# Kernel tuning notes

Hardware: AMD Instinct MI355X
Metric: run time of the kernel (lower is better)

## Reference

```python
import jax, jax.numpy as jnp
import numpy as np

B, T, INPUT_DIM = 4, 2048, 256
D_MODEL = 512                       # hidden_dim // 2
EXPAND = 2
D_INNER = D_MODEL * EXPAND          # 1024
HEADDIM = 128                       # _pick_headdim(1024)
NHEADS = D_INNER // HEADDIM         # 8
DSTATE = 16
DCONV = 4
NLAYERS = 4
CONV_DIM = D_INNER + 2 * DSTATE            # 1056
D_IN_PROJ = 2 * D_INNER + 2 * DSTATE + NHEADS  # 2088
EPS = 1e-5


def _dir_params(key):
    ks = jax.random.split(key, 5)
    return dict(
        in_w=jax.random.normal(ks[0], (NLAYERS, D_IN_PROJ, D_MODEL)) * 0.02,
        conv_w=jax.random.normal(ks[1], (NLAYERS, CONV_DIM, DCONV)) * 0.1,
        conv_b=jnp.zeros((NLAYERS, CONV_DIM)),
        dt_bias=jnp.log(jnp.expm1(jax.random.uniform(ks[2], (NLAYERS, NHEADS), minval=1e-3, maxval=0.1))),
        A_log=jnp.log(jax.random.uniform(ks[3], (NLAYERS, NHEADS), minval=1.0, maxval=16.0)),
        D=jnp.ones((NLAYERS, NHEADS)),
        rms_w=jnp.ones((NLAYERS, D_INNER)),
        out_w=jax.random.normal(ks[4], (NLAYERS, D_MODEL, D_INNER)) * 0.02,
    )


def setup_inputs():
    key = jax.random.key(0)
    kx, ke, kf, kb = jax.random.split(key, 4)
    inp = {
        "x": jax.random.normal(kx, (B, T, INPUT_DIM), dtype=jnp.float32),
        "embed_w": jax.random.normal(ke, (D_MODEL, INPUT_DIM)) * 0.02,
        "embed_b": jnp.zeros((D_MODEL,)),
        "ln1_w": jnp.ones((D_MODEL,)), "ln1_b": jnp.zeros((D_MODEL,)),
        "lnout_w": jnp.ones((2 * D_MODEL,)), "lnout_b": jnp.zeros((2 * D_MODEL,)),
    }
    for tag, p in (("f", _dir_params(kf)), ("b", _dir_params(kb))):
        for k, v in p.items():
            inp[f"{k}_{tag}"] = v
    return inp


def _silu(x):
    return x * jax.nn.sigmoid(x)


def _layernorm(x, w, b):
    m = jnp.mean(x, -1, keepdims=True)
    v = jnp.mean((x - m) ** 2, -1, keepdims=True)
    return (x - m) * jax.lax.rsqrt(v + EPS) * w + b


def _mamba2(h, in_w, conv_w, conv_b, dt_bias, A_log, Dh, rms_w, out_w):
    """One Mamba2 (SSD) block: in_proj -> causal depthwise conv -> selective scan
    -> gated RMSNorm -> out_proj. Sequential scan is math-equivalent to the
    chunked SSD kernel."""
    Bb, Tt, _ = h.shape
    zxbcdt = jnp.einsum('btd,ed->bte', h, in_w)
    z = zxbcdt[..., :D_INNER]
    xBC = zxbcdt[..., D_INNER:D_INNER + CONV_DIM]
    dt = zxbcdt[..., D_INNER + CONV_DIM:]                      # [B,T,H]
    # causal depthwise conv over time (kernel DCONV), then silu
    xc = jax.lax.conv_general_dilated(
        jnp.transpose(xBC, (0, 2, 1)), conv_w[:, None, :], (1,),
        [(DCONV - 1, 0)], feature_group_count=CONV_DIM)
    xBC = _silu(jnp.transpose(xc, (0, 2, 1)) + conv_b)
    xs = xBC[..., :D_INNER].reshape(Bb, Tt, NHEADS, HEADDIM)   # [B,T,H,P]
    Bm = xBC[..., D_INNER:D_INNER + DSTATE]                    # [B,T,N]
    Cm = xBC[..., D_INNER + DSTATE:]                           # [B,T,N]
    dt = jax.nn.softplus(dt + dt_bias)                         # [B,T,H]
    dA = jnp.exp(dt * (-jnp.exp(A_log)))                       # [B,T,H]
    xdt = xs * dt[..., None]                                   # [B,T,H,P]
    tm = lambda a: jnp.moveaxis(a, 1, 0)                       # time-major

    def step(s, inp):
        dA_t, xdt_t, B_t, C_t = inp
        s = dA_t[:, :, None, None] * s + xdt_t[..., None] * B_t[:, None, None, :]
        return s, jnp.einsum('bhpn,bn->bhp', s, C_t)

    s0 = jnp.zeros((Bb, NHEADS, HEADDIM, DSTATE), h.dtype)
    _, ys = jax.lax.scan(step, s0, (tm(dA), tm(xdt), tm(Bm), tm(Cm)))
    y = jnp.moveaxis(ys, 0, 1) + Dh[None, None, :, None] * xs
    y = y.reshape(Bb, Tt, D_INNER)
    g = y * _silu(z)                                           # gated RMSNorm (norm after gate)
    g = g * jax.lax.rsqrt(jnp.mean(g * g, -1, keepdims=True) + EPS) * rms_w
    return jnp.einsum('bti,oi->bto', g, out_w)


def _forward(x, embed_w, embed_b, ln1_w, ln1_b, lnout_w, lnout_b,
             in_w_f, conv_w_f, conv_b_f, dt_bias_f, A_log_f, D_f, rms_w_f, out_w_f,
             in_w_b, conv_w_b, conv_b_b, dt_bias_b, A_log_b, D_b, rms_w_b, out_w_b):
    h = _layernorm(jnp.einsum('bti,oi->bto', x, embed_w) + embed_b, ln1_w, ln1_b)
    h_f, h_b = h, h[:, ::-1]
    for i in range(NLAYERS):
        h_f = _mamba2(h_f, in_w_f[i], conv_w_f[i], conv_b_f[i], dt_bias_f[i],
                      A_log_f[i], D_f[i], rms_w_f[i], out_w_f[i]) + h_f
    for i in range(NLAYERS):
        h_b = _mamba2(h_b, in_w_b[i], conv_w_b[i], conv_b_b[i], dt_bias_b[i],
                      A_log_b[i], D_b[i], rms_w_b[i], out_w_b[i]) + h_b
    out = jnp.concatenate([h_f, h_b[:, ::-1]], axis=-1)        # [B,T,2*D_MODEL]
    return _layernorm(out, lnout_w, lnout_b)


def reference(x, embed_w, embed_b, ln1_w, ln1_b, lnout_w, lnout_b,
              in_w_f, conv_w_f, conv_b_f, dt_bias_f, A_log_f, D_f, rms_w_f, out_w_f,
              in_w_b, conv_w_b, conv_b_b, dt_bias_b, A_log_b, D_b, rms_w_b, out_w_b):
    return _forward(x, embed_w, embed_b, ln1_w, ln1_b, lnout_w, lnout_b,
                    in_w_f, conv_w_f, conv_b_f, dt_bias_f, A_log_f, D_f, rms_w_f, out_w_f,
                    in_w_b, conv_w_b, conv_b_b, dt_bias_b, A_log_b, D_b, rms_w_b, out_w_b)
```

## Files before the change

### kernel.cpp

```cpp
#include <hip/hip_runtime.h>
#include <hip/hip_bf16.h>
#include <math.h>

#define BB 4
#define TT 2048
#define BT 8192
#define DM 512
#define DI 1024
#define NH 8
#define HD 128
#define DS 16
#define CONVD 1056
#define DPROJ 2088
#define NL 4
#define CL 128
#define NCH 16
#define NE 131072

typedef __hip_bfloat16 bf16;
typedef __attribute__((ext_vector_type(8))) short short8;
typedef __attribute__((ext_vector_type(4))) short short4v;
typedef __attribute__((ext_vector_type(4))) float f32x4;

#define AS_G __attribute__((address_space(1)))
#define AS_L __attribute__((address_space(3)))

static __device__ __forceinline__ float b2f_raw(short v){
  union { unsigned u; float f; } c; c.u = ((unsigned)(unsigned short)v) << 16; return c.f;
}
static __device__ __forceinline__ float u32_lo(unsigned u){
  union { unsigned u; float f; } c; c.u = u << 16; return c.f;
}
static __device__ __forceinline__ float u32_hi(unsigned u){
  union { unsigned u; float f; } c; c.u = u & 0xffff0000u; return c.f;
}
static __device__ __forceinline__ unsigned pack_bf16x2(float a, float b){
  unsigned lo = __bfloat16_as_ushort(__float2bfloat16(a));
  unsigned hi = __bfloat16_as_ushort(__float2bfloat16(b));
  return lo | (hi << 16);
}

static __device__ __forceinline__ void red2(float& a, float& b, float* sb){
  #pragma unroll
  for (int o = 32; o; o >>= 1){ a += __shfl_down(a, o); b += __shfl_down(b, o); }
  int w = threadIdx.x >> 6;
  if ((threadIdx.x & 63) == 0){ sb[w] = a; sb[4+w] = b; }
  __syncthreads();
  a = sb[0]+sb[1]+sb[2]+sb[3];
  b = sb[4]+sb[5]+sb[6]+sb[7];
}

__global__ __launch_bounds__(256) void detect_dtype(const void* x, int* flagp){
  __shared__ int cnt;
  if (threadIdx.x == 0) cnt = 0;
  __syncthreads();
  const bf16* p = (const bf16*)x;
  int bad = 0;
  for (int i = threadIdx.x; i < 32768; i += 256){
    float v = __bfloat162float(p[i]);
    if (!isfinite(v) || fabsf(v) > 1e4f) bad++;
  }
  atomicAdd(&cnt, bad);
  __syncthreads();
  if (threadIdx.x == 0) *flagp = (cnt > 100) ? 1 : 0;
}

__global__ __launch_bounds__(256) void convert_in(const void* src, bf16* dst, int n,
                                                  const int* flagp){
  int f = *flagp;
  for (int i = blockIdx.x*256 + threadIdx.x; i < n; i += gridDim.x*256){
    if (f) dst[i] = __float2bfloat16(((const float*)src)[i]);
    else   dst[i] = ((const bf16*)src)[i];
  }
}

template<int OP>
__global__ __launch_bounds__(256,3) void gemm_nt(
    const bf16* __restrict__ A, const bf16* __restrict__ W0, const bf16* __restrict__ W1,
    bf16* C, const bf16* X, const float* __restrict__ srow,
    const bf16* db0, const bf16* db1, const bf16* al0, const bf16* al1,
    float2* __restrict__ dadt,
    int M, int N, int K, int lda, long sA, long sC)
{
  const int z = blockIdx.z;
  const bf16* Az = A + (long)z * sA;
  const bf16* W = z ? W1 : W0;
  const int m0 = blockIdx.x * 128, n0 = blockIdx.y * 128;
  __shared__ __align__(16) bf16 As[128*64];
  __shared__ __align__(16) bf16 Bs[128*64];
  const int tid  = threadIdx.x;
  const int lane = tid & 63, wv = tid >> 6;
  const int wm = wv >> 1, wn = wv & 1;
  const int quad = lane >> 4, l16 = lane & 15;
  const int srw = lane >> 3;
  const int skb = (lane & 7) * 16;

  f32x4 acc[4][4];
  #pragma unroll
  for (int i=0;i<4;i++)
    #pragma unroll
    for (int j=0;j<4;j++) acc[i][j] = (f32x4){0.f,0.f,0.f,0.f};

  for (int k0 = 0; k0 < K; k0 += 64){
    __syncthreads();
    #pragma unroll
    for (int is = 0; is < 4; ++is){
      int r = is*32 + wv*8 + srw;
      const char* gA = (const char*)(Az + (long)(m0 + r)*lda + k0) + skb;
      char* lA = (char*)As + (long)(is*32 + wv*8)*128;
      __builtin_amdgcn_global_load_lds((const AS_G void*)gA, (AS_L void*)lA, 16, 0, 0);
      int rn = n0 + r; rn = rn < N ? rn : N-1;
      const char* gB = (const char*)(W + (long)rn*K + k0) + skb;
      char* lB = (char*)Bs + (long)(is*32 + wv*8)*128;
      __builtin_amdgcn_global_load_lds((const AS_G void*)gB, (AS_L void*)lB, 16, 0, 0);
    }
    __syncthreads();
    #pragma unroll
    for (int sk = 0; sk < 2; ++sk){
      short8 af[4], bfr[4];
      #pragma unroll
      for (int mi=0;mi<4;mi++)  af[mi]  = *(const short8*)((const char*)As + (long)(wm*64+mi*16+l16)*128 + sk*64 + quad*16);
      #pragma unroll
      for (int ni=0;ni<4;ni++) bfr[ni] = *(const short8*)((const char*)Bs + (long)(wn*64+ni*16+l16)*128 + sk*64 + quad*16);
      #pragma unroll
      for (int mi=0;mi<4;mi++)
        #pragma unroll
        for (int ni=0;ni<4;ni++)
          acc[mi][ni] = __builtin_amdgcn_mfma_f32_16x16x32_bf16(af[mi], bfr[ni], acc[mi][ni], 0, 0, 0);
    }
  }

  bf16* Cz = C + (long)z * sC;
  const bf16* Xz = (OP==4) ? (X + (long)z * sC) : X;
  const bf16* db = z ? db1 : db0;
  const bf16* al = z ? al1 : al0;
  #pragma unroll
  for (int mi=0;mi<4;mi++){
    #pragma unroll
    for (int ni=0;ni<4;ni++){
      #pragma unroll
      for (int r=0;r<4;r++){
        int row = m0 + wm*64 + mi*16 + quad*4 + r;
        int col = n0 + wn*64 + ni*16 + l16;
        if (col < N){
          float v = acc[mi][ni][r];
          if (OP==1) v += __bfloat162float(X[col]);
          if (OP==4){
            v = v * srow[(long)z*BT + row] + __bfloat162float(Xz[(long)row*N + col]);
          }
          Cz[(long)row*N + col] = __float2bfloat16(v);
          if (OP==3 && col >= DPROJ-8){
            int h = col - (DPROJ-8), b = row >> 11, t = row & 2047;
            float xv = v + __bfloat162float(db[h]);
            float sp = (xv > 20.f) ? xv : log1pf(expf(xv));
            float da = expf(-expf(__bfloat162float(al[h])) * sp);
            float2 dd; dd.x = da; dd.y = sp;
            dadt[((long)(z*BB + b)*NH + h)*TT + t] = dd;
          }
        }
      }
    }
  }
}

__global__ __launch_bounds__(256) void embed_ln(const bf16* __restrict__ hp,
    const bf16* __restrict__ w, const bf16* __restrict__ bb, bf16* __restrict__ h)
{
  __shared__ float sb[8];
  int bt = blockIdx.x; int b = bt >> 11, t = bt & 2047;
  const bf16* r = hp + (long)bt*DM;
  int c0 = threadIdx.x, c1 = threadIdx.x + 256;
  float v0 = __bfloat162float(r[c0]);
  float v1 = __bfloat162float(r[c1]);
  float s = v0+v1, ss = v0*v0+v1*v1;
  red2(s, ss, sb);
  float m = s / DM;
  float var = ss / DM - m*m;
  float rs = rsqrtf(fmaxf(var, 0.f) + 1e-5f);
  float a0 = (v0-m)*rs*__bfloat162float(w[c0]) + __bfloat162float(bb[c0]);
  float a1 = (v1-m)*rs*__bfloat162float(w[c1]) + __bfloat162float(bb[c1]);
  bf16* o0 = h + (long)bt*DM;
  bf16* o1 = h + ((long)BT + (long)b*TT + (TT-1-t)) * DM;
  o0[c0] = __float2bfloat16(a0); o0[c1] = __float2bfloat16(a1);
  o1[c0] = __float2bfloat16(a0); o1[c1] = __float2bfloat16(a1);
}

__global__ __launch_bounds__(256) void conv_silu(const bf16* __restrict__ zx,
    const bf16* __restrict__ cw0, const bf16* __restrict__ cw1,
    const bf16* __restrict__ cb0, const bf16* __restrict__ cb1,
    bf16* __restrict__ xbc)
{
  int bt = blockIdx.x, dir = blockIdx.y;
  int t = bt & 2047;
  const bf16* cw = dir ? cw1 : cw0;
  const bf16* cb = dir ? cb1 : cb0;
  const bf16* zr = zx + ((long)dir*BT + bt)*DPROJ + DI;
  bf16* orow = xbc + ((long)dir*BT + bt)*CONVD;
  for (int cg = threadIdx.x; cg < CONVD/4; cg += 256){
    int c = cg*4;
    short8 w01 = *(const short8*)(cw + c*4);
    short8 w23 = *(const short8*)(cw + c*4 + 8);
    short4v bi = *(const short4v*)(cb + c);
    float acc[4];
    #pragma unroll
    for (int k=0;k<4;k++) acc[k] = b2f_raw(bi[k]);
    #pragma unroll
    for (int j=0;j<4;j++){
      if (t - 3 + j >= 0){
        short4v xv = *(const short4v*)(zr + (long)(j-3)*DPROJ + c);
        acc[0] = fmaf(b2f_raw(w01[j]),   b2f_raw(xv[0]), acc[0]);
        acc[1] = fmaf(b2f_raw(w01[4+j]), b2f_raw(xv[1]), acc[1]);
        acc[2] = fmaf(b2f_raw(w23[j]),   b2f_raw(xv[2]), acc[2]);
        acc[3] = fmaf(b2f_raw(w23[4+j]), b2f_raw(xv[3]), acc[3]);
      }
    }
    short4v ov;
    #pragma unroll
    for (int k=0;k<4;k++){
      float sg = 1.f / (1.f + expf(-acc[k]));
      ov[k] = (short)__bfloat16_as_ushort(__float2bfloat16(acc[k] * sg));
    }
    *(short4v*)(orow + c) = ov;
  }
}

#define CLG_LOAD(G, T0) do{ \
  _Pragma("unroll") \
  for (int _i=0;_i<4;_i++){ \
    const bf16* _rr = xr + (long)((T0)+_i)*CONVD; \
    G##x[_i]  = *(const unsigned*)(_rr + xoff); \
    G##B0[_i] = *(const short8*)(_rr + DI); \
    G##B1[_i] = *(const short8*)(_rr + DI + 8); \
    G##d[_i]  = ddr[(T0)+_i]; \
  } }while(0)

#define CLG_STEP(G) do{ \
  _Pragma("unroll") \
  for (int _i=0;_i<4;_i++){ \
    float _da = G##d[_i].x, _dt = G##d[_i].y; \
    float _x0 = u32_lo(G##x[_i]), _x1 = u32_hi(G##x[_i]); \
    float _xd0 = _x0*_dt, _xd1 = _x1*_dt; \
    _Pragma("unroll") \
    for (int _n=0;_n<8;_n++){ \
      float _b = b2f_raw(G##B0[_i][_n]); \
      s0[_n] = fmaf(_da, s0[_n], _xd0*_b); \
      s1[_n] = fmaf(_da, s1[_n], _xd1*_b); \
      float _b2 = b2f_raw(G##B1[_i][_n]); \
      s0[8+_n] = fmaf(_da, s0[8+_n], _xd0*_b2); \
      s1[8+_n] = fmaf(_da, s1[8+_n], _xd1*_b2); \
    } \
    pacc *= _da; \
  } }while(0)

#define CAG_LOAD(G, T0) do{ \
  _Pragma("unroll") \
  for (int _i=0;_i<4;_i++){ \
    const bf16* _rr = xr + (long)((T0)+_i)*CONVD; \
    G##x[_i]  = *(const unsigned*)(_rr + xoff); \
    G##B0[_i] = *(const short8*)(_rr + DI); \
    G##B1[_i] = *(const short8*)(_rr + DI + 8); \
    G##C0[_i] = *(const short8*)(_rr + DI + DS); \
    G##C1[_i] = *(const short8*)(_rr + DI + DS + 8); \
    G##z[_i]  = *(const unsigned*)(zr + (long)((T0)+_i)*DPROJ + xoff); \
    G##d[_i]  = ddr[(T0)+_i]; \
  } }while(0)

#define CAG_STEP(G, T0) do{ \
  _Pragma("unroll") \
  for (int _i=0;_i<4;_i++){ \
    float _da = G##d[_i].x, _dt = G##d[_i].y; \
    float _x0 = u32_lo(G##x[_i]), _x1 = u32_hi(G##x[_i]); \
    float _xd0 = _x0*_dt, _xd1 = _x1*_dt; \
    float _a0 = 0.f, _a1 = 0.f; \
    _Pragma("unroll") \
    for (int _n=0;_n<8;_n++){ \
      float _b = b2f_raw(G##B0[_i][_n]); \
      float _c = b2f_raw(G##C0[_i][_n]); \
      s0[_n] = fmaf(_da, s0[_n], _xd0*_b); \
      s1[_n] = fmaf(_da, s1[_n], _xd1*_b); \
      _a0 = fmaf(s0[_n], _c, _a0); \
      _a1 = fmaf(s1[_n], _c, _a1); \
      float _b2 = b2f_raw(G##B1[_i][_n]); \
      float _c2 = b2f_raw(G##C1[_i][_n]); \
      s0[8+_n] = fmaf(_da, s0[8+_n], _xd0*_b2); \
      s1[8+_n] = fmaf(_da, s1[8+_n], _xd1*_b2); \
      _a0 = fmaf(s0[8+_n], _c2, _a0); \
      _a1 = fmaf(s1[8+_n], _c2, _a1); \
    } \
    float _y0 = _a0 + Dv*_x0, _y1 = _a1 + Dv*_x1; \
    float _z0 = u32_lo(G##z[_i]), _z1 = u32_hi(G##z[_i]); \
    float _g0 = _y0 * _z0 / (1.f + expf(-_z0)); \
    float _g1 = _y1 * _z1 / (1.f + expf(-_z1)); \
    *(unsigned*)(zw + (long)((T0)+_i)*DPROJ + xoff) = pack_bf16x2(_g0, _g1); \
    float _pt = _g0*_g0 + _g1*_g1; \
    _Pragma("unroll") \
    for (int _o=1;_o<64;_o<<=1) _pt += __shfl_xor(_pt, _o); \
    if (lane == 0) gss[(long)dbh*TT + (T0)+_i] = _pt; \
  } }while(0)

__global__ __launch_bounds__(256,1) void chunk_local(const bf16* __restrict__ xbc,
    const float2* __restrict__ dadt, float* __restrict__ SC, float* __restrict__ Pc)
{
  int c = blockIdx.x;
  int dbh = blockIdx.y*4 + (threadIdx.x >> 6);
  int lane = threadIdx.x & 63;
  int dir = dbh >> 5, b = (dbh >> 3) & 3, h = dbh & 7;
  const bf16* xr = xbc + ((long)dir*BT + (long)b*TT) * CONVD;
  const float2* ddr = dadt + (long)dbh*TT;
  const int xoff = h*HD + lane*2;
  float s0[16], s1[16];
  #pragma unroll
  for (int n=0;n<16;n++){ s0[n]=0.f; s1[n]=0.f; }
  float pacc = 1.f;
  const int c0 = c*CL;

  unsigned Ax[4], Bx[4]; short8 AB0[4], AB1[4], BB0[4], BB1[4]; float2 Ad[4], Bd[4];
  CLG_LOAD(A, c0);
  for (int t0 = c0; t0 < c0+CL; t0 += 8){
    CLG_LOAD(B, t0+4);
    CLG_STEP(A);
    if (t0+8 < c0+CL) CLG_LOAD(A, t0+8);
    CLG_STEP(B);
  }
  float* sc = SC + (long)c*NE + (long)dbh*2048 + lane*32;
  #pragma unroll
  for (int n=0;n<16;n++){ sc[n] = s0[n]; sc[16+n] = s1[n]; }
  if (lane == 0) Pc[dbh*NCH + c] = pacc;
}

__global__ __launch_bounds__(256) void chunk_combine(float* __restrict__ SC,
    const float* __restrict__ Pc)
{
  int e = blockIdx.x*256 + threadIdx.x;
  int dbh = e >> 11;
  float s = 0.f;
  #pragma unroll
  for (int c=0;c<NCH;c++){
    float tmp = SC[(long)c*NE + e];
    SC[(long)c*NE + e] = s;
    s = Pc[dbh*NCH + c]*s + tmp;
  }
}

__global__ __launch_bounds__(256,1) void chunk_apply(const bf16* __restrict__ xbc,
    bf16* zx, const float2* __restrict__ dadt, const float* __restrict__ SC,
    const bf16* __restrict__ D0, const bf16* __restrict__ D1,
    float* __restrict__ gss)
{
  int c = blockIdx.x;
  int dbh = blockIdx.y*4 + (threadIdx.x >> 6);
  int lane = threadIdx.x & 63;
  int dir = dbh >> 5, b = (dbh >> 3) & 3, h = dbh & 7;
  const bf16* xr = xbc + ((long)dir*BT + (long)b*TT) * CONVD;
  const bf16* zr = zx + ((long)dir*BT + (long)b*TT) * DPROJ;
  bf16* zw = zx + ((long)dir*BT + (long)b*TT) * DPROJ;
  const float2* ddr = dadt + (long)dbh*TT;
  const int xoff = h*HD + lane*2;
  float Dv = __bfloat162float(dir ? D1[h] : D0[h]);
  const float* sc = SC + (long)c*NE + (long)dbh*2048 + lane*32;
  float s0[16], s1[16];
  #pragma unroll
  for (int n=0;n<16;n++){ s0[n] = sc[n]; s1[n] = sc[16+n]; }
  const int c0 = c*CL;

  unsigned Ax[4], Bx[4], Az_[4], Bz_[4];
  short8 AB0[4], AB1[4], BB0[4], BB1[4], AC0[4], AC1[4], BC0[4], BC1[4];
  float2 Ad[4], Bd[4];
  #define Az Az_
  #define Bz Bz_
  CAG_LOAD(A, c0);
  for (int t0 = c0; t0 < c0+CL; t0 += 8){
    CAG_LOAD(B, t0+4);
    CAG_STEP(A, t0);
    if (t0+8 < c0+CL) CAG_LOAD(A, t0+8);
    CAG_STEP(B, t0+4);
  }
  #undef Az
  #undef Bz
}

__global__ __launch_bounds__(256) void row_scale(const float* __restrict__ gss,
    float* __restrict__ srow)
{
  int i = blockIdx.x*256 + threadIdx.x;
  int dir = i >> 13, rem = i & 8191, b = rem >> 11, t = rem & 2047;
  int base = dir*32 + b*8;
  float s = 0.f;
  #pragma unroll
  for (int h=0;h<8;h++) s += gss[(long)(base+h)*TT + t];
  srow[i] = rsqrtf(s / DI + 1e-5f);
}

__global__ __launch_bounds__(256) void wg_scale(const bf16* __restrict__ w0,
    const bf16* __restrict__ w1, const bf16* __restrict__ r0,
    const bf16* __restrict__ r1, bf16* __restrict__ wg)
{
  int i = blockIdx.x*256 + threadIdx.x;
  int z = i >= DM*DI; int rem = z ? i - DM*DI : i;
  int col = rem & (DI-1);
  const bf16* w = z ? w1 : w0; const bf16* r = z ? r1 : r0;
  wg[i] = __float2bfloat16(__bfloat162float(w[rem]) * __bfloat162float(r[col]));
}

__global__ __launch_bounds__(256) void final_ln(const bf16* __restrict__ h,
    const bf16* __restrict__ lw, const bf16* __restrict__ lb, void* out,
    int mode, const int* flagp)
{
  __shared__ float sb[8];
  int bt = blockIdx.x; int b = bt >> 11, t = bt & 2047;
  int f32out = mode ? *flagp : 0;
  const bf16* rf = h + (long)bt*DM;
  const bf16* rb = h + ((long)BT + (long)b*TT + (TT-1-t))*DM;
  float v[4], s = 0.f, ss = 0.f;
  #pragma unroll
  for (int i=0;i<4;i++){
    int c = threadIdx.x + i*256;
    v[i] = __bfloat162float(c < DM ? rf[c] : rb[c-DM]);
    s += v[i]; ss += v[i]*v[i];
  }
  red2(s, ss, sb);
  float m = s / (2*DM);
  float var = ss / (2*DM) - m*m;
  float rs = rsqrtf(fmaxf(var, 0.f) + 1e-5f);
  #pragma unroll
  for (int i=0;i<4;i++){
    int c = threadIdx.x + i*256;
    float o = (v[i]-m)*rs*__bfloat162float(lw[c]) + __bfloat162float(lb[c]);
    if (f32out) ((float*)out)[(long)bt*(2*DM) + c] = o;
    else        ((bf16*)out)[(long)bt*(2*DM) + c] = __float2bfloat16(o);
  }
}

extern "C" void kernel_launch(void* const* d_in, const int* in_sizes, int n_in,
                              void* d_out, int out_size, void* d_ws, size_t ws_size,
                              hipStream_t stream)
{
  char* wsp = (char*)d_ws;
  auto take = [&](size_t bytes){ char* p = wsp; wsp += (bytes + 63) & ~(size_t)63; return p; };
  int*   flagp = (int*)  take(4);
  bf16*  h     = (bf16*) take((size_t)2*BT*DM*2);
  bf16*  zx    = (bf16*) take((size_t)2*BT*DPROJ*2);
  bf16*  xbc   = (bf16*) take((size_t)2*BT*CONVD*2);
  float2* dadt = (float2*)take((size_t)2*BB*NH*TT*8);
  float* gss   = (float*)take((size_t)2*BB*NH*TT*4);
  float* srowb = (float*)take((size_t)2*BT*4);
  float* Pc    = (float*)take((size_t)64*NCH*4);
  float* SC    = (float*)take((size_t)NCH*NE*4);
  bf16*  wg    = (bf16*)SC;
  size_t needDirect = (size_t)(wsp - (char*)d_ws);

  static const int cnt[23] = {
    BT*256, DM*256, DM, DM, DM, 2*DM, 2*DM,
    NL*DPROJ*DM, NL*CONVD*4, NL*CONVD, NL*NH, NL*NH, NL*NH, NL*DI, NL*DM*DI,
    NL*DPROJ*DM, NL*CONVD*4, NL*CONVD, NL*NH, NL*NH, NL*NH, NL*DI, NL*DM*DI };
  bf16* canon[23];
  for (int i = 0; i < 23; ++i) canon[i] = (bf16*)take((size_t)cnt[i]*2);
  size_t needFull = (size_t)(wsp - (char*)d_ws);

  const int convMode = (ws_size >= needFull) ? 1 : 0;

  const bf16* in[23];
  if (convMode){
    detect_dtype<<<1,256,0,stream>>>(d_in[0], flagp);
    for (int i = 0; i < 23; ++i){
      int grid = (cnt[i] + 255)/256; if (grid > 2048) grid = 2048;
      convert_in<<<grid,256,0,stream>>>(d_in[i], canon[i], cnt[i], flagp);
      in[i] = canon[i];
    }
  } else {
    for (int i = 0; i < 23; ++i) in[i] = (const bf16*)d_in[i];
  }

  const bf16* x       = in[0];
  const bf16* embed_w = in[1];
  const bf16* embed_b = in[2];
  const bf16* ln1_w   = in[3];
  const bf16* ln1_b   = in[4];
  const bf16* lnout_w = in[5];
  const bf16* lnout_b = in[6];
  const bf16* in_w[2]   = {in[7],  in[15]};
  const bf16* conv_w[2] = {in[8],  in[16]};
  const bf16* conv_b[2] = {in[9],  in[17]};
  const bf16* dt_b[2]   = {in[10], in[18]};
  const bf16* A_log[2]  = {in[11], in[19]};
  const bf16* Dp[2]     = {in[12], in[20]};
  const bf16* rms_w[2]  = {in[13], in[21]};
  const bf16* out_w[2]  = {in[14], in[22]};

  bf16* hpre = xbc;

  gemm_nt<1><<<dim3(64,4,1),256,0,stream>>>(x, embed_w, embed_w, hpre, embed_b,
      nullptr, nullptr, nullptr, nullptr, nullptr, nullptr,
      BT, DM, 256, 256, 0, 0);
  embed_ln<<<dim3(BT),256,0,stream>>>(hpre, ln1_w, ln1_b, h);

  for (int i = 0; i < NL; ++i){
    gemm_nt<3><<<dim3(64,17,2),256,0,stream>>>(h,
        in_w[0]+(size_t)i*DPROJ*DM, in_w[1]+(size_t)i*DPROJ*DM,
        zx, nullptr, nullptr,
        dt_b[0]+i*NH, dt_b[1]+i*NH, A_log[0]+i*NH, A_log[1]+i*NH, dadt,
        BT, DPROJ, DM, DM, (long)BT*DM, (long)BT*DPROJ);
    conv_silu<<<dim3(BT,2),256,0,stream>>>(zx,
        conv_w[0]+(size_t)i*CONVD*4, conv_w[1]+(size_t)i*CONVD*4,
        conv_b[0]+(size_t)i*CONVD, conv_b[1]+(size_t)i*CONVD, xbc);
    chunk_local<<<dim3(NCH,16),256,0,stream>>>(xbc, dadt, SC, Pc);
    chunk_combine<<<dim3(NE/256),256,0,stream>>>(SC, Pc);
    chunk_apply<<<dim3(NCH,16),256,0,stream>>>(xbc, zx, dadt, SC,
        Dp[0]+i*NH, Dp[1]+i*NH, gss);
    row_scale<<<dim3(2*BT/256),256,0,stream>>>(gss, srowb);
    wg_scale<<<dim3(2*DM*DI/256),256,0,stream>>>(out_w[0]+(size_t)i*DM*DI,
        out_w[1]+(size_t)i*DM*DI, rms_w[0]+(size_t)i*DI, rms_w[1]+(size_t)i*DI, wg);
    gemm_nt<4><<<dim3(64,4,2),256,0,stream>>>(zx, wg, wg+(size_t)DM*DI,
        h, h, srowb, nullptr, nullptr, nullptr, nullptr, nullptr,
        BT, DM, DI, DPROJ, (long)BT*DPROJ, (long)BT*DM);
  }

  final_ln<<<dim3(BT),256,0,stream>>>(h, lnout_w, lnout_b, d_out, convMode, flagp);
  (void)needDirect; (void)in_sizes; (void)n_in; (void)out_size;
}
```

Before: 1.291 ms.

## Swizzle GEMM LDS layout, split scan channels per lane, recompute RMS from zx

```diff
diff --git a/kernel.cpp b/kernel.cpp
--- a/kernel.cpp
+++ b/kernel.cpp
@@ -28,17 +28,6 @@
 static __device__ __forceinline__ float b2f_raw(short v){
   union { unsigned u; float f; } c; c.u = ((unsigned)(unsigned short)v) << 16; return c.f;
 }
-static __device__ __forceinline__ float u32_lo(unsigned u){
-  union { unsigned u; float f; } c; c.u = u << 16; return c.f;
-}
-static __device__ __forceinline__ float u32_hi(unsigned u){
-  union { unsigned u; float f; } c; c.u = u & 0xffff0000u; return c.f;
-}
-static __device__ __forceinline__ unsigned pack_bf16x2(float a, float b){
-  unsigned lo = __bfloat16_as_ushort(__float2bfloat16(a));
-  unsigned hi = __bfloat16_as_ushort(__float2bfloat16(b));
-  return lo | (hi << 16);
-}
 
 static __device__ __forceinline__ void red2(float& a, float& b, float* sb){
   #pragma unroll
@@ -92,8 +81,6 @@
   const int lane = tid & 63, wv = tid >> 6;
   const int wm = wv >> 1, wn = wv & 1;
   const int quad = lane >> 4, l16 = lane & 15;
-  const int srw = lane >> 3;
-  const int skb = (lane & 7) * 16;
 
   f32x4 acc[4][4];
   #pragma unroll
@@ -105,13 +92,15 @@
     __syncthreads();
     #pragma unroll
     for (int is = 0; is < 4; ++is){
-      int r = is*32 + wv*8 + srw;
-      const char* gA = (const char*)(Az + (long)(m0 + r)*lda + k0) + skb;
-      char* lA = (char*)As + (long)(is*32 + wv*8)*128;
+      int s  = wv*4 + is;
+      int rb = s >> 1, kb = s & 1;
+      int rA = m0 + rb*16 + l16;
+      const char* gA = (const char*)(Az + (long)rA*lda + k0 + kb*32 + quad*8);
+      char* lA = (char*)As + s*1024;
       __builtin_amdgcn_global_load_lds((const AS_G void*)gA, (AS_L void*)lA, 16, 0, 0);
-      int rn = n0 + r; rn = rn < N ? rn : N-1;
-      const char* gB = (const char*)(W + (long)rn*K + k0) + skb;
-      char* lB = (char*)Bs + (long)(is*32 + wv*8)*128;
+      int rB = n0 + rb*16 + l16; rB = rB < N ? rB : N-1;
+      const char* gB = (const char*)(W + (long)rB*K + k0 + kb*32 + quad*8);
+      char* lB = (char*)Bs + s*1024;
       __builtin_amdgcn_global_load_lds((const AS_G void*)gB, (AS_L void*)lB, 16, 0, 0);
     }
     __syncthreads();
@@ -119,9 +108,11 @@
     for (int sk = 0; sk < 2; ++sk){
       short8 af[4], bfr[4];
       #pragma unroll
-      for (int mi=0;mi<4;mi++)  af[mi]  = *(const short8*)((const char*)As + (long)(wm*64+mi*16+l16)*128 + sk*64 + quad*16);
+      for (int mi=0;mi<4;mi++)
+        af[mi]  = *(const short8*)((const char*)As + ((wm*4+mi)*2 + sk)*1024 + lane*16);
       #pragma unroll
-      for (int ni=0;ni<4;ni++) bfr[ni] = *(const short8*)((const char*)Bs + (long)(wn*64+ni*16+l16)*128 + sk*64 + quad*16);
+      for (int ni=0;ni<4;ni++)
+        bfr[ni] = *(const short8*)((const char*)Bs + ((wn*4+ni)*2 + sk)*1024 + lane*16);
       #pragma unroll
       for (int mi=0;mi<4;mi++)
         #pragma unroll
@@ -224,108 +215,62 @@
   }
 }
 
-#define CLG_LOAD(G, T0) do{ \
-  _Pragma("unroll") \
-  for (int _i=0;_i<4;_i++){ \
-    const bf16* _rr = xr + (long)((T0)+_i)*CONVD; \
-    G##x[_i]  = *(const unsigned*)(_rr + xoff); \
-    G##B0[_i] = *(const short8*)(_rr + DI); \
-    G##B1[_i] = *(const short8*)(_rr + DI + 8); \
-    G##d[_i]  = ddr[(T0)+_i]; \
-  } }while(0)
-
-#define CLG_STEP(G) do{ \
-  _Pragma("unroll") \
-  for (int _i=0;_i<4;_i++){ \
-    float _da = G##d[_i].x, _dt = G##d[_i].y; \
-    float _x0 = u32_lo(G##x[_i]), _x1 = u32_hi(G##x[_i]); \
-    float _xd0 = _x0*_dt, _xd1 = _x1*_dt; \
-    _Pragma("unroll") \
-    for (int _n=0;_n<8;_n++){ \
-      float _b = b2f_raw(G##B0[_i][_n]); \
-      s0[_n] = fmaf(_da, s0[_n], _xd0*_b); \
-      s1[_n] = fmaf(_da, s1[_n], _xd1*_b); \
-      float _b2 = b2f_raw(G##B1[_i][_n]); \
-      s0[8+_n] = fmaf(_da, s0[8+_n], _xd0*_b2); \
-      s1[8+_n] = fmaf(_da, s1[8+_n], _xd1*_b2); \
-    } \
-    pacc *= _da; \
-  } }while(0)
-
-#define CAG_LOAD(G, T0) do{ \
-  _Pragma("unroll") \
-  for (int _i=0;_i<4;_i++){ \
-    const bf16* _rr = xr + (long)((T0)+_i)*CONVD; \
-    G##x[_i]  = *(const unsigned*)(_rr + xoff); \
-    G##B0[_i] = *(const short8*)(_rr + DI); \
-    G##B1[_i] = *(const short8*)(_rr + DI + 8); \
-    G##C0[_i] = *(const short8*)(_rr + DI + DS); \
-    G##C1[_i] = *(const short8*)(_rr + DI + DS + 8); \
-    G##z[_i]  = *(const unsigned*)(zr + (long)((T0)+_i)*DPROJ + xoff); \
-    G##d[_i]  = ddr[(T0)+_i]; \
-  } }while(0)
-
-#define CAG_STEP(G, T0) do{ \
-  _Pragma("unroll") \
-  for (int _i=0;_i<4;_i++){ \
-    float _da = G##d[_i].x, _dt = G##d[_i].y; \
-    float _x0 = u32_lo(G##x[_i]), _x1 = u32_hi(G##x[_i]); \
-    float _xd0 = _x0*_dt, _xd1 = _x1*_dt; \
-    float _a0 = 0.f, _a1 = 0.f; \
-    _Pragma("unroll") \
-    for (int _n=0;_n<8;_n++){ \
-      float _b = b2f_raw(G##B0[_i][_n]); \
-      float _c = b2f_raw(G##C0[_i][_n]); \
-      s0[_n] = fmaf(_da, s0[_n], _xd0*_b); \
-      s1[_n] = fmaf(_da, s1[_n], _xd1*_b); \
-      _a0 = fmaf(s0[_n], _c, _a0); \
-      _a1 = fmaf(s1[_n], _c, _a1); \
-      float _b2 = b2f_raw(G##B1[_i][_n]); \
-      float _c2 = b2f_raw(G##C1[_i][_n]); \
-      s0[8+_n] = fmaf(_da, s0[8+_n], _xd0*_b2); \
-      s1[8+_n] = fmaf(_da, s1[8+_n], _xd1*_b2); \
-      _a0 = fmaf(s0[8+_n], _c2, _a0); \
-      _a1 = fmaf(s1[8+_n], _c2, _a1); \
-    } \
-    float _y0 = _a0 + Dv*_x0, _y1 = _a1 + Dv*_x1; \
-    float _z0 = u32_lo(G##z[_i]), _z1 = u32_hi(G##z[_i]); \
-    float _g0 = _y0 * _z0 / (1.f + expf(-_z0)); \
-    float _g1 = _y1 * _z1 / (1.f + expf(-_z1)); \
-    *(unsigned*)(zw + (long)((T0)+_i)*DPROJ + xoff) = pack_bf16x2(_g0, _g1); \
-    float _pt = _g0*_g0 + _g1*_g1; \
-    _Pragma("unroll") \
-    for (int _o=1;_o<64;_o<<=1) _pt += __shfl_xor(_pt, _o); \
-    if (lane == 0) gss[(long)dbh*TT + (T0)+_i] = _pt; \
-  } }while(0)
-
 __global__ __launch_bounds__(256,1) void chunk_local(const bf16* __restrict__ xbc,
     const float2* __restrict__ dadt, float* __restrict__ SC, float* __restrict__ Pc)
 {
   int c = blockIdx.x;
-  int dbh = blockIdx.y*4 + (threadIdx.x >> 6);
-  int lane = threadIdx.x & 63;
+  int wv = threadIdx.x >> 6, lane = threadIdx.x & 63;
+  int dbh = blockIdx.y*2 + (wv >> 1);
+  int ph  = wv & 1;
   int dir = dbh >> 5, b = (dbh >> 3) & 3, h = dbh & 7;
-  const bf16* xr = xbc + ((long)dir*BT + (long)b*TT) * CONVD;
+  const bf16* xr = xbc + ((long)dir*BT + (long)b*TT)*CONVD;
   const float2* ddr = dadt + (long)dbh*TT;
-  const int xoff = h*HD + lane*2;
-  float s0[16], s1[16];
-  #pragma unroll
-  for (int n=0;n<16;n++){ s0[n]=0.f; s1[n]=0.f; }
+  const int xoff = h*HD + ph*64 + lane;
+  float s[16];
+  #pragma unroll
+  for (int n=0;n<16;n++) s[n] = 0.f;
   float pacc = 1.f;
   const int c0 = c*CL;
 
-  unsigned Ax[4], Bx[4]; short8 AB0[4], AB1[4], BB0[4], BB1[4]; float2 Ad[4], Bd[4];
-  CLG_LOAD(A, c0);
+  float  gx[2][4];
+  short8 gB0[2][4], gB1[2][4];
+  float2 gd[2][4];
+
+  auto LOADG = [&](int buf, int t0){
+    #pragma unroll
+    for (int i=0;i<4;i++){
+      const bf16* rr = xr + (long)(t0+i)*CONVD;
+      gx[buf][i]  = __bfloat162float(rr[xoff]);
+      gB0[buf][i] = *(const short8*)(rr + DI);
+      gB1[buf][i] = *(const short8*)(rr + DI + 8);
+      gd[buf][i]  = ddr[t0+i];
+    }
+  };
+  auto STEPG = [&](int buf){
+    #pragma unroll
+    for (int i=0;i<4;i++){
+      float da = gd[buf][i].x, dt = gd[buf][i].y;
+      float xd = gx[buf][i]*dt;
+      #pragma unroll
+      for (int n=0;n<8;n++){
+        s[n]   = fmaf(da, s[n],   xd*b2f_raw(gB0[buf][i][n]));
+        s[8+n] = fmaf(da, s[8+n], xd*b2f_raw(gB1[buf][i][n]));
+      }
+      pacc *= da;
+    }
+  };
+
+  LOADG(0, c0);
   for (int t0 = c0; t0 < c0+CL; t0 += 8){
-    CLG_LOAD(B, t0+4);
-    CLG_STEP(A);
-    if (t0+8 < c0+CL) CLG_LOAD(A, t0+8);
-    CLG_STEP(B);
-  }
-  float* sc = SC + (long)c*NE + (long)dbh*2048 + lane*32;
-  #pragma unroll
-  for (int n=0;n<16;n++){ sc[n] = s0[n]; sc[16+n] = s1[n]; }
-  if (lane == 0) Pc[dbh*NCH + c] = pacc;
+    LOADG(1, t0+4);
+    STEPG(0);
+    if (t0+8 < c0+CL) LOADG(0, t0+8);
+    STEPG(1);
+  }
+  float* sc = SC + (long)c*NE + (long)dbh*2048 + ph*1024 + lane*16;
+  #pragma unroll
+  for (int n=0;n<16;n++) sc[n] = s[n];
+  if (ph == 0 && lane == 0) Pc[dbh*NCH + c] = pacc;
 }
 
 __global__ __launch_bounds__(256) void chunk_combine(float* __restrict__ SC,
@@ -344,51 +289,87 @@
 
 __global__ __launch_bounds__(256,1) void chunk_apply(const bf16* __restrict__ xbc,
     bf16* zx, const float2* __restrict__ dadt, const float* __restrict__ SC,
-    const bf16* __restrict__ D0, const bf16* __restrict__ D1,
-    float* __restrict__ gss)
+    const bf16* __restrict__ D0, const bf16* __restrict__ D1)
 {
   int c = blockIdx.x;
-  int dbh = blockIdx.y*4 + (threadIdx.x >> 6);
+  int wv = threadIdx.x >> 6, lane = threadIdx.x & 63;
+  int dbh = blockIdx.y*2 + (wv >> 1);
+  int ph  = wv & 1;
+  int dir = dbh >> 5, b = (dbh >> 3) & 3, h = dbh & 7;
+  const bf16* xr = xbc + ((long)dir*BT + (long)b*TT)*CONVD;
+  bf16* zrow = zx + ((long)dir*BT + (long)b*TT)*DPROJ;
+  const float2* ddr = dadt + (long)dbh*TT;
+  const int xoff = h*HD + ph*64 + lane;
+  float Dv = __bfloat162float(dir ? D1[h] : D0[h]);
+  const float* sc = SC + (long)c*NE + (long)dbh*2048 + ph*1024 + lane*16;
+  float s[16];
+  #pragma unroll
+  for (int n=0;n<16;n++) s[n] = sc[n];
+  const int c0 = c*CL;
+
+  float  gx[2][4], gz[2][4];
+  short8 gB0[2][4], gB1[2][4], gC0[2][4], gC1[2][4];
+  float2 gd[2][4];
+
+  auto LOADG = [&](int buf, int t0){
+    #pragma unroll
+    for (int i=0;i<4;i++){
+      const bf16* rr = xr + (long)(t0+i)*CONVD;
+      gx[buf][i]  = __bfloat162float(rr[xoff]);
+      gB0[buf][i] = *(const short8*)(rr + DI);
+      gB1[buf][i] = *(const short8*)(rr + DI + 8);
+      gC0[buf][i] = *(const short8*)(rr + DI + DS);
+      gC1[buf][i] = *(const short8*)(rr + DI + DS + 8);
+      gz[buf][i]  = __bfloat162float(zrow[(long)(t0+i)*DPROJ + xoff]);
+      gd[buf][i]  = ddr[t0+i];
+    }
+  };
+  auto STEPG = [&](int buf, int t0){
+    #pragma unroll
+    for (int i=0;i<4;i++){
+      float da = gd[buf][i].x, dt = gd[buf][i].y;
+      float xd = gx[buf][i]*dt;
+      float a = 0.f;
+      #pragma unroll
+      for (int n=0;n<8;n++){
+        s[n]   = fmaf(da, s[n],   xd*b2f_raw(gB0[buf][i][n]));
+        a      = fmaf(s[n],   b2f_raw(gC0[buf][i][n]), a);
+        s[8+n] = fmaf(da, s[8+n], xd*b2f_raw(gB1[buf][i][n]));
+        a      = fmaf(s[8+n], b2f_raw(gC1[buf][i][n]), a);
+      }
+      float y = a + Dv*gx[buf][i];
+      float zv = gz[buf][i];
+      float g = y * zv / (1.f + expf(-zv));
+      zrow[(long)(t0+i)*DPROJ + xoff] = __float2bfloat16(g);
+    }
+  };
+
+  LOADG(0, c0);
+  for (int t0 = c0; t0 < c0+CL; t0 += 8){
+    LOADG(1, t0+4);
+    STEPG(0, t0);
+    if (t0+8 < c0+CL) LOADG(0, t0+8);
+    STEPG(1, t0+4);
+  }
+}
+
+__global__ __launch_bounds__(256) void row_scale(const bf16* __restrict__ zx,
+    float* __restrict__ srow)
+{
+  int row = blockIdx.x*4 + (threadIdx.x >> 6);
   int lane = threadIdx.x & 63;
-  int dir = dbh >> 5, b = (dbh >> 3) & 3, h = dbh & 7;
-  const bf16* xr = xbc + ((long)dir*BT + (long)b*TT) * CONVD;
-  const bf16* zr = zx + ((long)dir*BT + (long)b*TT) * DPROJ;
-  bf16* zw = zx + ((long)dir*BT + (long)b*TT) * DPROJ;
-  const float2* ddr = dadt + (long)dbh*TT;
-  const int xoff = h*HD + lane*2;
-  float Dv = __bfloat162float(dir ? D1[h] : D0[h]);
-  const float* sc = SC + (long)c*NE + (long)dbh*2048 + lane*32;
-  float s0[16], s1[16];
-  #pragma unroll
-  for (int n=0;n<16;n++){ s0[n] = sc[n]; s1[n] = sc[16+n]; }
-  const int c0 = c*CL;
-
-  unsigned Ax[4], Bx[4], Az_[4], Bz_[4];
-  short8 AB0[4], AB1[4], BB0[4], BB1[4], AC0[4], AC1[4], BC0[4], BC1[4];
-  float2 Ad[4], Bd[4];
-  #define Az Az_
-  #define Bz Bz_
-  CAG_LOAD(A, c0);
-  for (int t0 = c0; t0 < c0+CL; t0 += 8){
-    CAG_LOAD(B, t0+4);
-    CAG_STEP(A, t0);
-    if (t0+8 < c0+CL) CAG_LOAD(A, t0+8);
-    CAG_STEP(B, t0+4);
-  }
-  #undef Az
-  #undef Bz
-}
-
-__global__ __launch_bounds__(256) void row_scale(const float* __restrict__ gss,
-    float* __restrict__ srow)
-{
-  int i = blockIdx.x*256 + threadIdx.x;
-  int dir = i >> 13, rem = i & 8191, b = rem >> 11, t = rem & 2047;
-  int base = dir*32 + b*8;
-  float s = 0.f;
-  #pragma unroll
-  for (int h=0;h<8;h++) s += gss[(long)(base+h)*TT + t];
-  srow[i] = rsqrtf(s / DI + 1e-5f);
+  const bf16* g = zx + (long)row*DPROJ + lane*16;
+  short8 a = *(const short8*)g;
+  short8 b = *(const short8*)(g + 8);
+  float ss = 0.f;
+  #pragma unroll
+  for (int k=0;k<8;k++){
+    float va = b2f_raw(a[k]), vb = b2f_raw(b[k]);
+    ss += va*va + vb*vb;
+  }
+  #pragma unroll
+  for (int o=1;o<64;o<<=1) ss += __shfl_xor(ss, o);
+  if (lane == 0) srow[row] = rsqrtf(ss / DI + 1e-5f);
 }
 
 __global__ __launch_bounds__(256) void wg_scale(const bf16* __restrict__ w0,
@@ -442,7 +423,6 @@
   bf16*  zx    = (bf16*) take((size_t)2*BT*DPROJ*2);
   bf16*  xbc   = (bf16*) take((size_t)2*BT*CONVD*2);
   float2* dadt = (float2*)take((size_t)2*BB*NH*TT*8);
-  float* gss   = (float*)take((size_t)2*BB*NH*TT*4);
   float* srowb = (float*)take((size_t)2*BT*4);
   float* Pc    = (float*)take((size_t)64*NCH*4);
   float* SC    = (float*)take((size_t)NCH*NE*4);
@@ -503,11 +483,11 @@
     conv_silu<<<dim3(BT,2),256,0,stream>>>(zx,
         conv_w[0]+(size_t)i*CONVD*4, conv_w[1]+(size_t)i*CONVD*4,
         conv_b[0]+(size_t)i*CONVD, conv_b[1]+(size_t)i*CONVD, xbc);
-    chunk_local<<<dim3(NCH,16),256,0,stream>>>(xbc, dadt, SC, Pc);
+    chunk_local<<<dim3(NCH,32),256,0,stream>>>(xbc, dadt, SC, Pc);
     chunk_combine<<<dim3(NE/256),256,0,stream>>>(SC, Pc);
-    chunk_apply<<<dim3(NCH,16),256,0,stream>>>(xbc, zx, dadt, SC,
-        Dp[0]+i*NH, Dp[1]+i*NH, gss);
-    row_scale<<<dim3(2*BT/256),256,0,stream>>>(gss, srowb);
+    chunk_apply<<<dim3(NCH,32),256,0,stream>>>(xbc, zx, dadt, SC,
+        Dp[0]+i*NH, Dp[1]+i*NH);
+    row_scale<<<dim3(2*BT/4),256,0,stream>>>(zx, srowb);
     wg_scale<<<dim3(2*DM*DI/256),256,0,stream>>>(out_w[0]+(size_t)i*DM*DI,
         out_w[1]+(size_t)i*DM*DI, rms_w[0]+(size_t)i*DI, rms_w[1]+(size_t)i*DI, wg);
     gemm_nt<4><<<dim3(64,4,2),256,0,stream>>>(zx, wg, wg+(size_t)DM*DI,
```

After: 1.325 ms. 2.6% more time.
